# Kernel tuning notes

Hardware: AMD Instinct MI355X
Metric: run time of the kernel (lower is better)

The kernel has to match this reference:

```python
import jax, jax.numpy as jnp
import numpy as np

B, C, H, W = 4, 64, 64, 64


def setup_inputs() -> dict:
    key = jax.random.key(0)
    ks = jax.random.split(key, 7)
    s = 1.0 / np.sqrt(C)
    return {
        "x": jax.random.normal(ks[0], (B, C, H, W), dtype=jnp.float32),
        "wq": jax.random.normal(ks[1], (C, C), dtype=jnp.float32) * s,
        "bq": jax.random.normal(ks[2], (C,), dtype=jnp.float32) * s,
        "wk": jax.random.normal(ks[3], (C, C), dtype=jnp.float32) * s,
        "bk": jax.random.normal(ks[4], (C,), dtype=jnp.float32) * s,
        "wv": jax.random.normal(ks[5], (C, C), dtype=jnp.float32) * s,
        "bv": jax.random.normal(ks[6], (C,), dtype=jnp.float32) * s,
    }


def reference(x, wq, bq, wk, bk, wv, bv):
    b, c, h, w = x.shape
    n = h * w
    xf = x.reshape(b, c, n)  # flatten spatial -> tokens
    # 1x1 convs == per-pixel linear projections over channels
    q = jnp.einsum('oc,bcn->bon', wq, xf) + bq[None, :, None]
    k = jnp.einsum('oc,bcn->bon', wk, xf) + bk[None, :, None]
    v = jnp.einsum('oc,bcn->bon', wv, xf) + bv[None, :, None]
    # attn[b,i,j] = sum_c q[b,c,i] k[b,c,j] / N   (note: scaled by N, as in source)
    attn = jnp.einsum('bci,bcj->bij', q, k) / n
    attn = jax.nn.softmax(attn, axis=-1)
    # out[b,c,i] = sum_j v[b,c,j] attn[i,j]  (v @ attn^T)
    out = jnp.einsum('bcj,bij->bci', v, attn)
    return out.reshape(b, c, h, w)
```

## Files before the change

### kernel.cpp

```cpp
#include <hip/hip_runtime.h>

#define CCH 64
#define NTOK 4096
#define NF 4096.0f
#define INVN 2.44140625e-4f


__global__ __launch_bounds__(256) void init_kernel(float* __restrict__ p) {
  int i = (blockIdx.x * 256 + threadIdx.x) * 4;
  if (i < 4 * 4096 + 2 * 4 * 64) {
    float4 z = {0.f, 0.f, 0.f, 0.f};
    *(float4*)&p[i] = z;
  }
}

__global__ __launch_bounds__(256) void mstats_kernel(
    const float* __restrict__ x,
    const float* __restrict__ wk, const float* __restrict__ bk,
    const float* __restrict__ wv, const float* __restrict__ bv,
    float* __restrict__ M, float* __restrict__ ksum, float* __restrict__ vsum)
{
  __shared__ __align__(16) float xs[64][68];
  __shared__ __align__(16) float WkS[64][68];
  __shared__ __align__(16) float WvS[64][68];
  __shared__ float bkS[64], bvS[64];

  const int tid = threadIdx.x;
  const int b = blockIdx.x >> 6, s = blockIdx.x & 63;
  const int n0 = s * 64;

  const float* xb = x + (size_t)b * CCH * NTOK + n0;
#pragma unroll
  for (int k = 0; k < 4; ++k) {
    int id = tid + k * 256;
    int r = id >> 4, c4 = (id & 15) * 4;
    *(float4*)&xs[r][c4]  = *(const float4*)(xb + (size_t)r * NTOK + c4);
    *(float4*)&WkS[r][c4] = *(const float4*)(wk + r * 64 + c4);
    *(float4*)&WvS[r][c4] = *(const float4*)(wv + r * 64 + c4);
  }
  if (tid < 64) { bkS[tid] = bk[tid]; bvS[tid] = bv[tid]; }
  __syncthreads();

  const int r0 = (tid >> 4) * 4, t0 = (tid & 15) * 4;

  float ak[4][4], av[4][4];
#pragma unroll
  for (int i = 0; i < 4; ++i)
#pragma unroll
    for (int j = 0; j < 4; ++j) { ak[i][j] = bkS[r0 + i]; av[i][j] = bvS[r0 + i]; }

  for (int c0 = 0; c0 < 64; c0 += 4) {
    float4 xv[4], wkr[4], wvr[4];
#pragma unroll
    for (int cc = 0; cc < 4; ++cc) xv[cc] = *(const float4*)&xs[c0 + cc][t0];
#pragma unroll
    for (int i = 0; i < 4; ++i) {
      wkr[i] = *(const float4*)&WkS[r0 + i][c0];
      wvr[i] = *(const float4*)&WvS[r0 + i][c0];
    }
#pragma unroll
    for (int i = 0; i < 4; ++i) {
      float wka[4] = {wkr[i].x, wkr[i].y, wkr[i].z, wkr[i].w};
      float wva[4] = {wvr[i].x, wvr[i].y, wvr[i].z, wvr[i].w};
#pragma unroll
      for (int cc = 0; cc < 4; ++cc) {
        float xa[4] = {xv[cc].x, xv[cc].y, xv[cc].z, xv[cc].w};
#pragma unroll
        for (int j = 0; j < 4; ++j) {
          ak[i][j] += wka[cc] * xa[j];
          av[i][j] += wva[cc] * xa[j];
        }
      }
    }
  }
  __syncthreads();

#pragma unroll
  for (int i = 0; i < 4; ++i)
#pragma unroll
    for (int j = 0; j < 4; ++j) {
      WkS[t0 + j][r0 + i] = ak[i][j];
      WvS[t0 + j][r0 + i] = av[i][j];
    }
  __syncthreads();

  float accM[4][4];
#pragma unroll
  for (int i = 0; i < 4; ++i)
#pragma unroll
    for (int j = 0; j < 4; ++j) accM[i][j] = 0.f;
#pragma unroll 8
  for (int t = 0; t < 64; ++t) {
    float4 vv = *(const float4*)&WvS[t][r0];
    float4 kk = *(const float4*)&WkS[t][t0];
    float va[4] = {vv.x, vv.y, vv.z, vv.w};
    float ka[4] = {kk.x, kk.y, kk.z, kk.w};
#pragma unroll
    for (int i = 0; i < 4; ++i)
#pragma unroll
      for (int j = 0; j < 4; ++j) accM[i][j] += va[i] * ka[j];
  }

  float* Mb = M + (size_t)b * 4096;
#pragma unroll
  for (int i = 0; i < 4; ++i)
#pragma unroll
    for (int j = 0; j < 4; ++j)
      atomicAdd(&Mb[(r0 + i) * 64 + t0 + j], accM[i][j]);

  if (tid < 64) {
    float sk = 0.f;
#pragma unroll 16
    for (int t = 0; t < 64; ++t) sk += WkS[t][tid];
    atomicAdd(&ksum[b * 64 + tid], sk);
  } else if (tid < 128) {
    int c = tid - 64;
    float sv = 0.f;
#pragma unroll 16
    for (int t = 0; t < 64; ++t) sv += WvS[t][c];
    atomicAdd(&vsum[b * 64 + c], sv);
  }
}

__global__ __launch_bounds__(256) void algebra_kernel(
    const float* __restrict__ M, const float* __restrict__ ksum,
    const float* __restrict__ vsum,
    const float* __restrict__ wq, const float* __restrict__ bq,
    float* __restrict__ Amat, float* __restrict__ c0v,
    float* __restrict__ wdv, float* __restrict__ d0v)
{
  __shared__ __align__(16) float Ms[64][68];
  __shared__ float Wqs[64][17];
  __shared__ float ksS[64], bqS[64];

  const int tid = threadIdx.x;
  const int b = blockIdx.x >> 2, js = blockIdx.x & 3;
  const int j0 = js * 16;

#pragma unroll
  for (int k = 0; k < 4; ++k) {
    int cell = (tid + k * 256) * 4;
    *(float4*)&Ms[cell >> 6][cell & 63] = *(const float4*)&M[(size_t)b * 4096 + cell];
    int id = tid + k * 256;
    int a = id >> 4, jl = id & 15;
    Wqs[a][jl] = wq[a * 64 + j0 + jl];
  }
  if (tid < 64) { ksS[tid] = ksum[b * 64 + tid]; bqS[tid] = bq[tid]; }
  __syncthreads();

  const int r0 = (tid >> 4) * 4, jl = tid & 15;
  float acc[4] = {0.f, 0.f, 0.f, 0.f};
  for (int a0 = 0; a0 < 64; a0 += 4) {
    float w4[4];
#pragma unroll
    for (int aa = 0; aa < 4; ++aa) w4[aa] = Wqs[a0 + aa][jl];
#pragma unroll
    for (int i = 0; i < 4; ++i) {
      float4 m = *(const float4*)&Ms[r0 + i][a0];
      acc[i] += m.x * w4[0] + m.y * w4[1] + m.z * w4[2] + m.w * w4[3];
    }
  }
#pragma unroll
  for (int i = 0; i < 4; ++i)
    Amat[(size_t)b * 4096 + (r0 + i) * 64 + j0 + jl] = acc[i] * INVN;

  if (js == 0) {
    if (tid < 64) {
      float s = 0.f;
      for (int a = 0; a < 64; ++a) s += wq[a * 64 + tid] * ksS[a];
      wdv[b * 64 + tid] = s * INVN;
    } else if (tid < 128) {
      int t = tid - 64;
      float s = 0.f;
      for (int a = 0; a < 64; ++a) s += Ms[t][a] * bqS[a];
      c0v[b * 64 + t] = vsum[b * 64 + t] + s * INVN;
    } else if (tid == 128) {
      float s = 0.f;
      for (int a = 0; a < 64; ++a) s += ksS[a] * bqS[a];
      d0v[b] = NF + s * INVN;
    }
  }
}

__global__ __launch_bounds__(256) void out_kernel(
    const float* __restrict__ x, const float* __restrict__ Amat,
    const float* __restrict__ c0v, const float* __restrict__ wdv,
    const float* __restrict__ d0v, float* __restrict__ out)
{
  __shared__ __align__(16) float xs[64][68];
  __shared__ __align__(16) float As[64][68];
  __shared__ __align__(16) float c0s[64], wds[64];
  __shared__ float d0s;
  const int tid = threadIdx.x;
  const int b = blockIdx.x >> 6, ck = blockIdx.x & 63;
  const int n0 = ck * 64;
  const float* xb = x + (size_t)b * CCH * NTOK + n0;
#pragma unroll
  for (int k = 0; k < 4; ++k) {
    int id = tid + k * 256;
    int c = id >> 4, t4 = (id & 15) * 4;
    *(float4*)&xs[c][t4] = *(const float4*)(xb + (size_t)c * NTOK + t4);
    *(float4*)&As[c][t4] = *(const float4*)(Amat + (size_t)b * 4096 + c * 64 + t4);
  }
  if (tid < 64) { c0s[tid] = c0v[b * 64 + tid]; wds[tid] = wdv[b * 64 + tid]; }
  if (tid == 0) d0s = d0v[b];
  __syncthreads();

  const int o0 = (tid >> 4) * 4, t0 = (tid & 15) * 4;
  float acc[4][4], den[4];
#pragma unroll
  for (int r = 0; r < 4; ++r)
#pragma unroll
    for (int j = 0; j < 4; ++j) acc[r][j] = 0.f;
#pragma unroll
  for (int j = 0; j < 4; ++j) den[j] = 0.f;

  for (int cq = 0; cq < 16; ++cq) {
    float xr[4][4], ar[4][4], wv4[4];
#pragma unroll
    for (int i = 0; i < 4; ++i) {
      float4 t = *(const float4*)&xs[cq * 4 + i][t0];
      xr[i][0] = t.x; xr[i][1] = t.y; xr[i][2] = t.z; xr[i][3] = t.w;
    }
#pragma unroll
    for (int r = 0; r < 4; ++r) {
      float4 t = *(const float4*)&As[o0 + r][cq * 4];
      ar[r][0] = t.x; ar[r][1] = t.y; ar[r][2] = t.z; ar[r][3] = t.w;
    }
    {
      float4 t = *(const float4*)&wds[cq * 4];
      wv4[0] = t.x; wv4[1] = t.y; wv4[2] = t.z; wv4[3] = t.w;
    }
#pragma unroll
    for (int i = 0; i < 4; ++i) {
#pragma unroll
      for (int j = 0; j < 4; ++j) den[j] += wv4[i] * xr[i][j];
#pragma unroll
      for (int r = 0; r < 4; ++r)
#pragma unroll
        for (int j = 0; j < 4; ++j) acc[r][j] += ar[r][i] * xr[i][j];
    }
  }
  const float dv = d0s;
  float inv[4];
#pragma unroll
  for (int j = 0; j < 4; ++j) inv[j] = 1.f / (den[j] + dv);
  float* ob = out + (size_t)b * CCH * NTOK + n0 + t0;
#pragma unroll
  for (int r = 0; r < 4; ++r) {
    float c0r = c0s[o0 + r];
    float4 res;
    res.x = (acc[r][0] + c0r) * inv[0];
    res.y = (acc[r][1] + c0r) * inv[1];
    res.z = (acc[r][2] + c0r) * inv[2];
    res.w = (acc[r][3] + c0r) * inv[3];
    *(float4*)(ob + (size_t)(o0 + r) * NTOK) = res;
  }
}

extern "C" void kernel_launch(void* const* d_in, const int* in_sizes, int n_in,
                              void* d_out, int out_size, void* d_ws, size_t ws_size,
                              hipStream_t stream) {
  const float* x  = (const float*)d_in[0];
  const float* wq = (const float*)d_in[1];
  const float* bq = (const float*)d_in[2];
  const float* wk = (const float*)d_in[3];
  const float* bk = (const float*)d_in[4];
  const float* wv = (const float*)d_in[5];
  const float* bv = (const float*)d_in[6];
  float* out = (float*)d_out;

  float* M    = (float*)d_ws;
  float* ksum = M + 4 * 4096;
  float* vsum = ksum + 4 * 64;
  float* Amat = vsum + 4 * 64;
  float* c0v  = Amat + 4 * 4096;
  float* wdv  = c0v + 4 * 64;
  float* d0v  = wdv + 4 * 64;

  hipLaunchKernelGGL(init_kernel, dim3(17), dim3(256), 0, stream, M);
  hipLaunchKernelGGL(mstats_kernel, dim3(256), dim3(256), 0, stream,
                     x, wk, bk, wv, bv, M, ksum, vsum);
  hipLaunchKernelGGL(algebra_kernel, dim3(16), dim3(256), 0, stream,
                     M, ksum, vsum, wq, bq, Amat, c0v, wdv, d0v);
  hipLaunchKernelGGL(out_kernel, dim3(256), dim3(256), 0, stream,
                     x, Amat, c0v, wdv, d0v, out);
}
```

Baseline: 101.0 us.

## Fuse all stages into one cooperative kernel with grid syncs and partial buffers

Replaces the four kernel launches with a single cooperative kernel that uses grid.sync between phases. Per-block partial results for M, ksum and vsum are written to workspace instead of atomically accumulated, then reduced by a subset of blocks. Each block recomputes the small Wq algebra locally so the separate algebra kernel goes away. The aim is to remove launch overhead and atomic contention, at the cost of grid-wide barriers, extra partial-buffer traffic (about 4 MB) and redundant per-block algebra.

```diff
diff --git a/kernel.cpp b/kernel.cpp
--- a/kernel.cpp
+++ b/kernel.cpp
@@ -1,4 +1,7 @@
 #include <hip/hip_runtime.h>
+#include <hip/hip_cooperative_groups.h>
+
+namespace cg = cooperative_groups;
 
 #define CCH 64
 #define NTOK 4096
@@ -6,42 +9,42 @@
 #define INVN 2.44140625e-4f
 
 
-__global__ __launch_bounds__(256) void init_kernel(float* __restrict__ p) {
-  int i = (blockIdx.x * 256 + threadIdx.x) * 4;
-  if (i < 4 * 4096 + 2 * 4 * 64) {
-    float4 z = {0.f, 0.f, 0.f, 0.f};
-    *(float4*)&p[i] = z;
-  }
-}
-
-__global__ __launch_bounds__(256) void mstats_kernel(
+__global__ __launch_bounds__(256) void fused_kernel(
     const float* __restrict__ x,
+    const float* __restrict__ wq, const float* __restrict__ bq,
     const float* __restrict__ wk, const float* __restrict__ bk,
     const float* __restrict__ wv, const float* __restrict__ bv,
-    float* __restrict__ M, float* __restrict__ ksum, float* __restrict__ vsum)
+    float* __restrict__ Mpart, float* __restrict__ kpart,
+    float* __restrict__ vpart, float* __restrict__ Mred,
+    float* __restrict__ ksum, float* __restrict__ vsum,
+    float* __restrict__ out)
 {
   __shared__ __align__(16) float xs[64][68];
-  __shared__ __align__(16) float WkS[64][68];
-  __shared__ __align__(16) float WvS[64][68];
+  __shared__ __align__(16) float B1[64][68];
+  __shared__ __align__(16) float B2[64][68];
   __shared__ float bkS[64], bvS[64];
+  __shared__ float ksS[64], vsS[64], bqS[64], wds[64], c0s[64];
+  __shared__ float d0s;
+
+  cg::grid_group grid = cg::this_grid();
 
   const int tid = threadIdx.x;
-  const int b = blockIdx.x >> 6, s = blockIdx.x & 63;
+  const int blk = blockIdx.x;
+  const int b = blk >> 6, s = blk & 63;
   const int n0 = s * 64;
+  const int r0 = (tid >> 4) * 4, t0 = (tid & 15) * 4;
 
   const float* xb = x + (size_t)b * CCH * NTOK + n0;
 #pragma unroll
   for (int k = 0; k < 4; ++k) {
     int id = tid + k * 256;
     int r = id >> 4, c4 = (id & 15) * 4;
-    *(float4*)&xs[r][c4]  = *(const float4*)(xb + (size_t)r * NTOK + c4);
-    *(float4*)&WkS[r][c4] = *(const float4*)(wk + r * 64 + c4);
-    *(float4*)&WvS[r][c4] = *(const float4*)(wv + r * 64 + c4);
+    *(float4*)&xs[r][c4] = *(const float4*)(xb + (size_t)r * NTOK + c4);
+    *(float4*)&B1[r][c4] = *(const float4*)(wk + r * 64 + c4);
+    *(float4*)&B2[r][c4] = *(const float4*)(wv + r * 64 + c4);
   }
   if (tid < 64) { bkS[tid] = bk[tid]; bvS[tid] = bv[tid]; }
   __syncthreads();
-
-  const int r0 = (tid >> 4) * 4, t0 = (tid & 15) * 4;
 
   float ak[4][4], av[4][4];
 #pragma unroll
@@ -55,8 +58,8 @@
     for (int cc = 0; cc < 4; ++cc) xv[cc] = *(const float4*)&xs[c0 + cc][t0];
 #pragma unroll
     for (int i = 0; i < 4; ++i) {
-      wkr[i] = *(const float4*)&WkS[r0 + i][c0];
-      wvr[i] = *(const float4*)&WvS[r0 + i][c0];
+      wkr[i] = *(const float4*)&B1[r0 + i][c0];
+      wvr[i] = *(const float4*)&B2[r0 + i][c0];
     }
 #pragma unroll
     for (int i = 0; i < 4; ++i) {
@@ -79,8 +82,8 @@
   for (int i = 0; i < 4; ++i)
 #pragma unroll
     for (int j = 0; j < 4; ++j) {
-      WkS[t0 + j][r0 + i] = ak[i][j];
-      WvS[t0 + j][r0 + i] = av[i][j];
+      B1[t0 + j][r0 + i] = ak[i][j];
+      B2[t0 + j][r0 + i] = av[i][j];
     }
   __syncthreads();
 
@@ -91,8 +94,8 @@
     for (int j = 0; j < 4; ++j) accM[i][j] = 0.f;
 #pragma unroll 8
   for (int t = 0; t < 64; ++t) {
-    float4 vv = *(const float4*)&WvS[t][r0];
-    float4 kk = *(const float4*)&WkS[t][t0];
+    float4 vv = *(const float4*)&B2[t][r0];
+    float4 kk = *(const float4*)&B1[t][t0];
     float va[4] = {vv.x, vv.y, vv.z, vv.w};
     float ka[4] = {kk.x, kk.y, kk.z, kk.w};
 #pragma unroll
@@ -100,113 +103,111 @@
 #pragma unroll
       for (int j = 0; j < 4; ++j) accM[i][j] += va[i] * ka[j];
   }
-
-  float* Mb = M + (size_t)b * 4096;
-#pragma unroll
-  for (int i = 0; i < 4; ++i)
-#pragma unroll
-    for (int j = 0; j < 4; ++j)
-      atomicAdd(&Mb[(r0 + i) * 64 + t0 + j], accM[i][j]);
-
+  float* mp = Mpart + ((size_t)blk << 12);
+#pragma unroll
+  for (int i = 0; i < 4; ++i) {
+    float4 v4; v4.x = accM[i][0]; v4.y = accM[i][1];
+    v4.z = accM[i][2]; v4.w = accM[i][3];
+    *(float4*)&mp[(r0 + i) * 64 + t0] = v4;
+  }
   if (tid < 64) {
     float sk = 0.f;
 #pragma unroll 16
-    for (int t = 0; t < 64; ++t) sk += WkS[t][tid];
-    atomicAdd(&ksum[b * 64 + tid], sk);
+    for (int t = 0; t < 64; ++t) sk += B1[t][tid];
+    kpart[blk * 64 + tid] = sk;
   } else if (tid < 128) {
     int c = tid - 64;
     float sv = 0.f;
 #pragma unroll 16
-    for (int t = 0; t < 64; ++t) sv += WvS[t][c];
-    atomicAdd(&vsum[b * 64 + c], sv);
-  }
-}
-
-__global__ __launch_bounds__(256) void algebra_kernel(
-    const float* __restrict__ M, const float* __restrict__ ksum,
-    const float* __restrict__ vsum,
-    const float* __restrict__ wq, const float* __restrict__ bq,
-    float* __restrict__ Amat, float* __restrict__ c0v,
-    float* __restrict__ wdv, float* __restrict__ d0v)
-{
-  __shared__ __align__(16) float Ms[64][68];
-  __shared__ float Wqs[64][17];
-  __shared__ float ksS[64], bqS[64];
-
-  const int tid = threadIdx.x;
-  const int b = blockIdx.x >> 2, js = blockIdx.x & 3;
-  const int j0 = js * 16;
-
-#pragma unroll
-  for (int k = 0; k < 4; ++k) {
-    int cell = (tid + k * 256) * 4;
-    *(float4*)&Ms[cell >> 6][cell & 63] = *(const float4*)&M[(size_t)b * 4096 + cell];
-    int id = tid + k * 256;
-    int a = id >> 4, jl = id & 15;
-    Wqs[a][jl] = wq[a * 64 + j0 + jl];
-  }
-  if (tid < 64) { ksS[tid] = ksum[b * 64 + tid]; bqS[tid] = bq[tid]; }
-  __syncthreads();
-
-  const int r0 = (tid >> 4) * 4, jl = tid & 15;
-  float acc[4] = {0.f, 0.f, 0.f, 0.f};
-  for (int a0 = 0; a0 < 64; a0 += 4) {
-    float w4[4];
-#pragma unroll
-    for (int aa = 0; aa < 4; ++aa) w4[aa] = Wqs[a0 + aa][jl];
-#pragma unroll
-    for (int i = 0; i < 4; ++i) {
-      float4 m = *(const float4*)&Ms[r0 + i][a0];
-      acc[i] += m.x * w4[0] + m.y * w4[1] + m.z * w4[2] + m.w * w4[3];
-    }
-  }
-#pragma unroll
-  for (int i = 0; i < 4; ++i)
-    Amat[(size_t)b * 4096 + (r0 + i) * 64 + j0 + jl] = acc[i] * INVN;
-
-  if (js == 0) {
+    for (int t = 0; t < 64; ++t) sv += B2[t][c];
+    vpart[blk * 64 + c] = sv;
+  }
+
+  __threadfence();
+  grid.sync();
+
+  if (blk < 128) {
+    int rb = blk >> 5, row0 = (blk & 31) * 2;
+    if (tid < 128) {
+      int row = row0 + (tid >> 6), col = tid & 63;
+      float sum = 0.f;
+      const float* src = Mpart + ((size_t)rb << 18) + row * 64 + col;
+      for (int sl = 0; sl < 64; ++sl) sum += src[(size_t)sl << 12];
+      Mred[rb * 4096 + row * 64 + col] = sum;
+    }
+  } else if (blk < 132) {
+    int rb = blk - 128;
     if (tid < 64) {
-      float s = 0.f;
-      for (int a = 0; a < 64; ++a) s += wq[a * 64 + tid] * ksS[a];
-      wdv[b * 64 + tid] = s * INVN;
+      float sk = 0.f;
+      for (int sl = 0; sl < 64; ++sl) sk += kpart[(rb * 64 + sl) * 64 + tid];
+      ksum[rb * 64 + tid] = sk;
     } else if (tid < 128) {
-      int t = tid - 64;
-      float s = 0.f;
-      for (int a = 0; a < 64; ++a) s += Ms[t][a] * bqS[a];
-      c0v[b * 64 + t] = vsum[b * 64 + t] + s * INVN;
-    } else if (tid == 128) {
-      float s = 0.f;
-      for (int a = 0; a < 64; ++a) s += ksS[a] * bqS[a];
-      d0v[b] = NF + s * INVN;
-    }
-  }
-}
-
-__global__ __launch_bounds__(256) void out_kernel(
-    const float* __restrict__ x, const float* __restrict__ Amat,
-    const float* __restrict__ c0v, const float* __restrict__ wdv,
-    const float* __restrict__ d0v, float* __restrict__ out)
-{
-  __shared__ __align__(16) float xs[64][68];
-  __shared__ __align__(16) float As[64][68];
-  __shared__ __align__(16) float c0s[64], wds[64];
-  __shared__ float d0s;
-  const int tid = threadIdx.x;
-  const int b = blockIdx.x >> 6, ck = blockIdx.x & 63;
-  const int n0 = ck * 64;
-  const float* xb = x + (size_t)b * CCH * NTOK + n0;
+      int c = tid - 64;
+      float sv = 0.f;
+      for (int sl = 0; sl < 64; ++sl) sv += vpart[(rb * 64 + sl) * 64 + c];
+      vsum[rb * 64 + c] = sv;
+    }
+  }
+
+  __threadfence();
+  grid.sync();
+
 #pragma unroll
   for (int k = 0; k < 4; ++k) {
     int id = tid + k * 256;
-    int c = id >> 4, t4 = (id & 15) * 4;
-    *(float4*)&xs[c][t4] = *(const float4*)(xb + (size_t)c * NTOK + t4);
-    *(float4*)&As[c][t4] = *(const float4*)(Amat + (size_t)b * 4096 + c * 64 + t4);
-  }
-  if (tid < 64) { c0s[tid] = c0v[b * 64 + tid]; wds[tid] = wdv[b * 64 + tid]; }
-  if (tid == 0) d0s = d0v[b];
-  __syncthreads();
-
-  const int o0 = (tid >> 4) * 4, t0 = (tid & 15) * 4;
+    int r = id >> 4, c4 = (id & 15) * 4;
+    *(float4*)&B1[r][c4] = *(const float4*)&Mred[b * 4096 + r * 64 + c4];
+    *(float4*)&B2[r][c4] = *(const float4*)(wq + r * 64 + c4);
+  }
+  if (tid < 64) { ksS[tid] = ksum[b * 64 + tid]; bqS[tid] = bq[tid]; }
+  else if (tid < 128) vsS[tid - 64] = vsum[b * 64 + tid - 64];
+  __syncthreads();
+
+  if (tid < 64) {
+    float sw = 0.f;
+    for (int a = 0; a < 64; ++a) sw += B2[a][tid] * ksS[a];
+    wds[tid] = sw * INVN;
+  } else if (tid < 128) {
+    int o = tid - 64;
+    float sc = 0.f;
+    for (int a = 0; a < 64; ++a) sc += B1[o][a] * bqS[a];
+    c0s[o] = vsS[o] + sc * INVN;
+  } else if (tid == 128) {
+    float sd = 0.f;
+    for (int a = 0; a < 64; ++a) sd += ksS[a] * bqS[a];
+    d0s = NF + sd * INVN;
+  }
+
+  const int col0 = t0;
+  float accA[4][4];
+#pragma unroll
+  for (int i = 0; i < 4; ++i)
+#pragma unroll
+    for (int j = 0; j < 4; ++j) accA[i][j] = 0.f;
+  for (int a0 = 0; a0 < 64; a0 += 4) {
+    float4 m4[4], w4[4];
+#pragma unroll
+    for (int i = 0; i < 4; ++i) m4[i] = *(const float4*)&B1[r0 + i][a0];
+#pragma unroll
+    for (int aa = 0; aa < 4; ++aa) w4[aa] = *(const float4*)&B2[a0 + aa][col0];
+#pragma unroll
+    for (int i = 0; i < 4; ++i) {
+      float ma[4] = {m4[i].x, m4[i].y, m4[i].z, m4[i].w};
+#pragma unroll
+      for (int aa = 0; aa < 4; ++aa) {
+        float wa[4] = {w4[aa].x, w4[aa].y, w4[aa].z, w4[aa].w};
+#pragma unroll
+        for (int j = 0; j < 4; ++j) accA[i][j] += ma[aa] * wa[j];
+      }
+    }
+  }
+  __syncthreads();
+#pragma unroll
+  for (int i = 0; i < 4; ++i)
+#pragma unroll
+    for (int j = 0; j < 4; ++j) B2[r0 + i][col0 + j] = accA[i][j] * INVN;
+  __syncthreads();
+
   float acc[4][4], den[4];
 #pragma unroll
   for (int r = 0; r < 4; ++r)
@@ -224,7 +225,7 @@
     }
 #pragma unroll
     for (int r = 0; r < 4; ++r) {
-      float4 t = *(const float4*)&As[o0 + r][cq * 4];
+      float4 t = *(const float4*)&B2[r0 + r][cq * 4];
       ar[r][0] = t.x; ar[r][1] = t.y; ar[r][2] = t.z; ar[r][3] = t.w;
     }
     {
@@ -248,13 +249,13 @@
   float* ob = out + (size_t)b * CCH * NTOK + n0 + t0;
 #pragma unroll
   for (int r = 0; r < 4; ++r) {
-    float c0r = c0s[o0 + r];
+    float c0r = c0s[r0 + r];
     float4 res;
     res.x = (acc[r][0] + c0r) * inv[0];
     res.y = (acc[r][1] + c0r) * inv[1];
     res.z = (acc[r][2] + c0r) * inv[2];
     res.w = (acc[r][3] + c0r) * inv[3];
-    *(float4*)(ob + (size_t)(o0 + r) * NTOK) = res;
+    *(float4*)(ob + (size_t)(r0 + r) * NTOK) = res;
   }
 }
 
@@ -270,19 +271,17 @@
   const float* bv = (const float*)d_in[6];
   float* out = (float*)d_out;
 
-  float* M    = (float*)d_ws;
-  float* ksum = M + 4 * 4096;
-  float* vsum = ksum + 4 * 64;
-  float* Amat = vsum + 4 * 64;
-  float* c0v  = Amat + 4 * 4096;
-  float* wdv  = c0v + 4 * 64;
-  float* d0v  = wdv + 4 * 64;
-
-  hipLaunchKernelGGL(init_kernel, dim3(17), dim3(256), 0, stream, M);
-  hipLaunchKernelGGL(mstats_kernel, dim3(256), dim3(256), 0, stream,
-                     x, wk, bk, wv, bv, M, ksum, vsum);
-  hipLaunchKernelGGL(algebra_kernel, dim3(16), dim3(256), 0, stream,
-                     M, ksum, vsum, wq, bq, Amat, c0v, wdv, d0v);
-  hipLaunchKernelGGL(out_kernel, dim3(256), dim3(256), 0, stream,
-                     x, Amat, c0v, wdv, d0v, out);
+  float* Mpart = (float*)d_ws;
+  float* kpart = Mpart + 256 * 4096;
+  float* vpart = kpart + 256 * 64;
+  float* Mred  = vpart + 256 * 64;
+  float* ksum  = Mred + 4 * 4096;
+  float* vsum  = ksum + 4 * 64;
+
+  void* args[] = {(void*)&x, (void*)&wq, (void*)&bq, (void*)&wk, (void*)&bk,
+                  (void*)&wv, (void*)&bv, (void*)&Mpart, (void*)&kpart,
+                  (void*)&vpart, (void*)&Mred, (void*)&ksum, (void*)&vsum,
+                  (void*)&out};
+  hipLaunchCooperativeKernel((void*)fused_kernel, dim3(256), dim3(256),
+                             args, 0, stream);
 }
```

Result: slower. 200.7 us (+98.6%).
